# Kernel optimization log

Measured on AMD Instinct MI355X. Metric: run time of the kernel, lower is better.

The kernel has to match this reference:

```python
import jax, jax.numpy as jnp
import numpy as np

N, D, C = 8192, 256, 100
MARGIN = 1.0


def setup_inputs() -> dict:
    key = jax.random.key(0)
    k1, k2 = jax.random.split(key)
    features = jax.random.normal(k1, (N, D), dtype=jnp.float32)
    labels = jax.random.randint(k2, (N,), 0, C, dtype=jnp.int64)
    return {"features": features, "labels": labels}


def _pairwise_dist(f):
    # f: [N, D] L2-normalized rows. Euclidean distance matrix [N, N].
    sq = jnp.sum(f * f, axis=1)  # [N]
    d2 = sq[:, None] + sq[None, :] - 2.0 * (f @ f.T)
    d2 = jnp.maximum(d2, 0.0)
    # safe sqrt: zero distance (incl. diagonal) -> 0 with finite grad
    pos = d2 > 0.0
    return jnp.where(pos, jnp.sqrt(jnp.where(pos, d2, 1.0)), 0.0)


def reference(features, labels):
    # F.normalize(p=2, dim=1)
    norm = jnp.linalg.norm(features, axis=1, keepdims=True)
    f = features / jnp.maximum(norm, 1e-12)

    dist = _pairwise_dist(f)  # [N, N]

    onehot = jax.nn.one_hot(labels, C, dtype=f.dtype)  # [N, C]
    counts = jnp.sum(onehot, axis=0)  # [C]
    # S[a, b] = sum_{i in a, j in b} dist[i, j]
    S = onehot.T @ dist @ onehot  # [C, C]

    # intra: per-class mean over off-diagonal pairs (diag of dist is 0),
    # only classes with count > 1, then mean over those classes
    intra_valid = counts > 1.0
    intra_denom = jnp.where(intra_valid, counts * (counts - 1.0), 1.0)
    intra_per_class = jnp.diag(S) / intra_denom
    n_intra = jnp.sum(intra_valid.astype(f.dtype))
    intra = jnp.where(
        n_intra > 0,
        jnp.sum(jnp.where(intra_valid, intra_per_class, 0.0)) / jnp.maximum(n_intra, 1.0),
        0.0,
    )

    # inter: per class-pair (a < b, both present) mean distance, then mean over pairs
    pair_cnt = counts[:, None] * counts[None, :]
    inter_mat = S / jnp.where(pair_cnt > 0.0, pair_cnt, 1.0)
    present = counts > 0.0
    upper = jnp.triu(jnp.ones((C, C), dtype=bool), k=1)
    pair_mask = upper & present[:, None] & present[None, :]
    n_pairs = jnp.sum(pair_mask.astype(f.dtype))
    inter = jnp.where(
        n_pairs > 0,
        jnp.sum(jnp.where(pair_mask, inter_mat, 0.0)) / jnp.maximum(n_pairs, 1.0),
        1.0,
    )

    loss = jax.nn.relu(intra - inter + MARGIN)
    return loss  # scalar; .mean() of a scalar is itself
```

## Files before the change

kernel.cpp:

```cpp
#include <hip/hip_runtime.h>
#include <math.h>

#define N_ROWS 8192
#define D_DIM  256
#define C_CLS  100
#define BM 128
#define BK 32
#define NSTRIP (N_ROWS / BM)
#define NBLK (NSTRIP * (NSTRIP + 1) / 2)
#define UPK (C_CLS * (C_CLS + 1) / 2)
#define NHB (N_ROWS / 256)
#define MAXSEG 4

typedef __attribute__((ext_vector_type(8))) __bf16 bf16x8;
typedef __attribute__((ext_vector_type(4))) float  floatx4;

__device__ __forceinline__ unsigned short f2bf(float x) {
    unsigned int u = __float_as_uint(x);
    u += 0x7fff + ((u >> 16) & 1);
    return (unsigned short)(u >> 16);
}

__device__ __forceinline__ void gl2lds16(const void* g, void* l) {
    __builtin_amdgcn_global_load_lds(
        (const __attribute__((address_space(1))) void*)g,
        (__attribute__((address_space(3))) void*)l, 16, 0, 0);
}

__global__ void hist_k(const int* __restrict__ labels, int* __restrict__ hist_part) {
    __shared__ int h[C_CLS];
    const int t = threadIdx.x;
    if (t < C_CLS) h[t] = 0;
    __syncthreads();
    atomicAdd(&h[labels[blockIdx.x * 256 + t]], 1);
    __syncthreads();
    if (t < C_CLS) hist_part[blockIdx.x * C_CLS + t] = h[t];
}

__global__ void scan_k(const int* __restrict__ hist_part, int* __restrict__ offs,
                       int* __restrict__ blockoffs, float* __restrict__ Ug) {
    __shared__ int tot[C_CLS];
    const int t = threadIdx.x;
    if (t < C_CLS) {
        int run = 0;
        for (int b = 0; b < NHB; ++b) {
            blockoffs[b * C_CLS + t] = run;
            run += hist_part[b * C_CLS + t];
        }
        tot[t] = run;
    }
    __syncthreads();
    if (t == 0) {
        int run = 0;
        for (int c = 0; c < C_CLS; ++c) { offs[c] = run; run += tot[c]; }
        offs[C_CLS] = run;
    }
    for (int e = t; e < UPK; e += 256) Ug[e] = 0.f;
}

__global__ void scatter_k(const int* __restrict__ labels, const int* __restrict__ offs,
                          const int* __restrict__ blockoffs, int* __restrict__ dest,
                          int* __restrict__ slab) {
    __shared__ int cur[C_CLS];
    const int t = threadIdx.x;
    if (t < C_CLS) cur[t] = offs[t] + blockoffs[blockIdx.x * C_CLS + t];
    __syncthreads();
    const int i  = blockIdx.x * 256 + t;
    const int la = labels[i];
    const int pos = atomicAdd(&cur[la], 1);
    dest[i] = pos;
    slab[pos] = la;
}

__global__ void normalize_k(const float* __restrict__ in, const int* __restrict__ dest,
                            unsigned short* __restrict__ fnb) {
    const int row  = blockIdx.x * 4 + (threadIdx.x >> 6);
    const int lane = threadIdx.x & 63;
    float4 v = ((const float4*)in)[row * 64 + lane];
    float s = v.x * v.x + v.y * v.y + v.z * v.z + v.w * v.w;
#pragma unroll
    for (int o = 32; o > 0; o >>= 1) s += __shfl_xor(s, o, 64);
    const float inv = 1.f / fmaxf(sqrtf(s), 1e-12f);
    const int d = dest[row];
    ushort4 o4;
    o4.x = f2bf(v.x * inv); o4.y = f2bf(v.y * inv);
    o4.z = f2bf(v.z * inv); o4.w = f2bf(v.w * inv);
    ((ushort4*)fnb)[d * 64 + lane] = o4;
}

__global__ __launch_bounds__(256, 4)
void main_k(const unsigned short* __restrict__ fnb, const int* __restrict__ slab,
            const int* __restrict__ offs_g, float* __restrict__ Ug) {
    __shared__ __align__(16) unsigned short As[BM * BK];
    __shared__ __align__(16) unsigned short Bs[BM * BK];
    __shared__ float red[4][MAXSEG * MAXSEG][65];
    __shared__ int soffs[C_CLS + 1];
    __shared__ int meta[4][4];

    const int t = threadIdx.x;

    int b = blockIdx.x, ti = 0, len = NSTRIP;
    while (b >= len) { b -= len; ++ti; --len; }
    const int tj = ti + b;
    const int i0 = ti * BM, j0 = tj * BM;

    if (t < C_CLS + 1) soffs[t] = offs_g[t];
    for (int e = t; e < 4 * MAXSEG * MAXSEG * 65; e += 256) (&red[0][0][0])[e] = 0.f;

    const int lane = t & 63;
    const int w    = t >> 6;
    const int m0 = (w & 1) * 64, n0 = (w >> 1) * 64;
    const int lr = lane & 15, lq = lane >> 4;
    const int swz = (lr >> 1) & 3;

    int aoff[4], boff[4];
#pragma unroll
    for (int mb = 0; mb < 4; ++mb) aoff[mb] = (m0 + mb * 16 + lr) * BK + ((lq ^ swz) * 8);
#pragma unroll
    for (int nb = 0; nb < 4; ++nb) boff[nb] = (n0 + nb * 16 + lr) * BK + ((lq ^ swz) * 8);

    const int s0 = t, s1 = t + 256;
    const int r0 = s0 >> 2, kc0 = (s0 & 3) ^ ((r0 >> 1) & 3);
    const int r1 = s1 >> 2, kc1 = (s1 & 3) ^ ((r1 >> 1) & 3);

    floatx4 acc[4][4];
#pragma unroll
    for (int mb = 0; mb < 4; ++mb)
#pragma unroll
        for (int nb = 0; nb < 4; ++nb) acc[mb][nb] = 0.f;

    for (int k0 = 0; k0 < D_DIM; k0 += BK) {
        __syncthreads();
        gl2lds16(&fnb[(size_t)(i0 + r0) * D_DIM + k0 + kc0 * 8], &As[s0 * 8]);
        gl2lds16(&fnb[(size_t)(i0 + r1) * D_DIM + k0 + kc1 * 8], &As[s1 * 8]);
        gl2lds16(&fnb[(size_t)(j0 + r0) * D_DIM + k0 + kc0 * 8], &Bs[s0 * 8]);
        gl2lds16(&fnb[(size_t)(j0 + r1) * D_DIM + k0 + kc1 * 8], &Bs[s1 * 8]);
        __syncthreads();

        bf16x8 a[4], bb[4];
#pragma unroll
        for (int mb = 0; mb < 4; ++mb) a[mb]  = *(const bf16x8*)&As[aoff[mb]];
#pragma unroll
        for (int nb = 0; nb < 4; ++nb) bb[nb] = *(const bf16x8*)&Bs[boff[nb]];
#pragma unroll
        for (int mb = 0; mb < 4; ++mb)
#pragma unroll
            for (int nb = 0; nb < 4; ++nb)
                acc[mb][nb] = __builtin_amdgcn_mfma_f32_16x16x32_bf16(a[mb], bb[nb], acc[mb][nb], 0, 0, 0);
    }

    const bool diag = (ti == tj);
#pragma unroll
    for (int mb = 0; mb < 4; ++mb)
#pragma unroll
        for (int nb = 0; nb < 4; ++nb)
#pragma unroll
            for (int r = 0; r < 4; ++r) {
                const float g = acc[mb][nb][r];
                float dv = __builtin_amdgcn_sqrtf(fmaxf(2.f - 2.f * g, 0.f));
                const int rt = m0 + mb * 16 + lq * 4 + r;
                const int ct = n0 + nb * 16 + lr;
                if (diag && rt == ct) dv = 0.f;
                acc[mb][nb][r] = dv;
            }

    const int cA0 = __builtin_amdgcn_readfirstlane(slab[i0 + m0]);
    const int cA1 = __builtin_amdgcn_readfirstlane(slab[i0 + m0 + 63]);
    const int cB0 = __builtin_amdgcn_readfirstlane(slab[j0 + n0]);
    const int cB1 = __builtin_amdgcn_readfirstlane(slab[j0 + n0 + 63]);
    const int segsA = cA1 - cA0 + 1, segsB = cB1 - cB0 + 1;
    if (lane == 0) { meta[w][0] = cA0; meta[w][1] = cB0; meta[w][2] = segsA; meta[w][3] = segsB; }
    const float wscale = diag ? 1.f : 2.f;

    float rem[4][4];
#pragma unroll
    for (int mb = 0; mb < 4; ++mb)
#pragma unroll
        for (int r = 0; r < 4; ++r)
            rem[mb][r] = acc[mb][0][r] + acc[mb][1][r] + acc[mb][2][r] + acc[mb][3][r];

    for (int sb = 0; sb < segsB; ++sb) {
        const int cb = cB0 + sb;
        float colsum[4][4];
        if (sb == segsB - 1) {
#pragma unroll
            for (int mb = 0; mb < 4; ++mb)
#pragma unroll
                for (int r = 0; r < 4; ++r) colsum[mb][r] = rem[mb][r];
        } else {
            const int rb0 = max(soffs[cb]     - j0, n0);
            const int rb1 = min(soffs[cb + 1] - j0, n0 + 64);
#pragma unroll
            for (int mb = 0; mb < 4; ++mb)
#pragma unroll
                for (int r = 0; r < 4; ++r) colsum[mb][r] = 0.f;
#pragma unroll
            for (int nb = 0; nb < 4; ++nb) {
                const int ct = n0 + nb * 16 + lr;
                const bool ic = (ct >= rb0) & (ct < rb1);
#pragma unroll
                for (int mb = 0; mb < 4; ++mb)
#pragma unroll
                    for (int r = 0; r < 4; ++r)
                        colsum[mb][r] += ic ? acc[mb][nb][r] : 0.f;
            }
#pragma unroll
            for (int mb = 0; mb < 4; ++mb)
#pragma unroll
                for (int r = 0; r < 4; ++r) rem[mb][r] -= colsum[mb][r];
        }
        for (int sa = 0; sa < segsA; ++sa) {
            const int ca = cA0 + sa;
            const int ra0 = max(soffs[ca]     - i0, m0);
            const int ra1 = min(soffs[ca + 1] - i0, m0 + 64);
            float v = 0.f;
#pragma unroll
            for (int mb = 0; mb < 4; ++mb) {
                const int rtb = m0 + mb * 16 + lq * 4;
#pragma unroll
                for (int r = 0; r < 4; ++r) {
                    const int rt = rtb + r;
                    const bool ir = (rt >= ra0) & (rt < ra1);
                    v += ir ? colsum[mb][r] : 0.f;
                }
            }
            if (sa < MAXSEG && sb < MAXSEG) {
                red[w][sb * MAXSEG + sa][lane] = v;
            } else {
#pragma unroll
                for (int o = 32; o > 0; o >>= 1) v += __shfl_xor(v, o, 64);
                if (lane == 0 && v != 0.f) {
                    const int mn = min(ca, cb), mx = max(ca, cb);
                    atomicAdd(&Ug[mx + ((mn * (2 * C_CLS - 1 - mn)) >> 1)], wscale * v);
                }
            }
        }
    }

    __syncthreads();
    {
        const int combo = t >> 2, q = t & 3;
        const int wv = combo >> 4, sl = combo & 15;
        float s = 0.f;
#pragma unroll
        for (int k = 0; k < 16; ++k) s += red[wv][sl][q * 16 + k];
        s += __shfl_xor(s, 1, 64);
        s += __shfl_xor(s, 2, 64);
        const int sa = sl & (MAXSEG - 1), sb = sl >> 2;
        if (q == 0 && sa < meta[wv][2] && sb < meta[wv][3] && s != 0.f) {
            const int ca = meta[wv][0] + sa, cb = meta[wv][1] + sb;
            const int mn = min(ca, cb), mx = max(ca, cb);
            atomicAdd(&Ug[mx + ((mn * (2 * C_CLS - 1 - mn)) >> 1)], wscale * s);
        }
    }
}

__global__ void finalize_k(const float* __restrict__ U, const int* __restrict__ offs,
                           float* __restrict__ out) {
    __shared__ int   cnt[C_CLS];
    __shared__ float rf[256];
    __shared__ int   ri[256];
    const int t = threadIdx.x;
    if (t < C_CLS) cnt[t] = offs[t + 1] - offs[t];
    __syncthreads();

    float s_intra = 0.f; int n_intra = 0;
    if (t < C_CLS) {
        int c = cnt[t];
        if (c > 1) {
            int idx = t + ((t * (2 * C_CLS - 1 - t)) >> 1);
            s_intra = U[idx] / ((float)c * (float)(c - 1));
            n_intra = 1;
        }
    }
    float s_inter = 0.f; int n_pairs = 0;
    for (int p = t; p < C_CLS * C_CLS; p += 256) {
        int a = p / C_CLS, b2 = p - a * C_CLS;
        if (b2 > a && cnt[a] > 0 && cnt[b2] > 0) {
            int idx = b2 + ((a * (2 * C_CLS - 1 - a)) >> 1);
            s_inter += 0.5f * U[idx] / ((float)cnt[a] * (float)cnt[b2]);
            ++n_pairs;
        }
    }

    rf[t] = s_intra; ri[t] = n_intra; __syncthreads();
    for (int s = 128; s > 0; s >>= 1) {
        if (t < s) { rf[t] += rf[t + s]; ri[t] += ri[t + s]; }
        __syncthreads();
    }
    float intra_sum = rf[0]; int intra_n = ri[0];
    __syncthreads();
    rf[t] = s_inter; ri[t] = n_pairs; __syncthreads();
    for (int s = 128; s > 0; s >>= 1) {
        if (t < s) { rf[t] += rf[t + s]; ri[t] += ri[t + s]; }
        __syncthreads();
    }
    if (t == 0) {
        float inter_sum = rf[0]; int pairs_n = ri[0];
        float intra = (intra_n > 0) ? intra_sum / (float)intra_n : 0.f;
        float inter = (pairs_n > 0) ? inter_sum / (float)pairs_n : 1.f;
        out[0] = fmaxf(intra - inter + 1.0f, 0.f);
    }
}

extern "C" void kernel_launch(void* const* d_in, const int* in_sizes, int n_in,
                              void* d_out, int out_size, void* d_ws, size_t ws_size,
                              hipStream_t stream) {
    const float* feats  = (const float*)d_in[0];
    const int*   labels = (const int*)d_in[1];
    float* out = (float*)d_out;

    char* p = (char*)d_ws;
    unsigned short* fnb = (unsigned short*)p;  p += (size_t)N_ROWS * D_DIM * sizeof(unsigned short);
    int*   slab      = (int*)p;  p += (size_t)N_ROWS * sizeof(int);
    int*   dest      = (int*)p;  p += (size_t)N_ROWS * sizeof(int);
    int*   hist_part = (int*)p;  p += (size_t)NHB * C_CLS * sizeof(int);
    int*   blockoffs = (int*)p;  p += (size_t)NHB * C_CLS * sizeof(int);
    int*   offs      = (int*)p;  p += 128 * sizeof(int);
    float* Ug        = (float*)p;

    hist_k    <<<NHB, 256, 0, stream>>>(labels, hist_part);
    scan_k    <<<1, 256, 0, stream>>>(hist_part, offs, blockoffs, Ug);
    scatter_k <<<NHB, 256, 0, stream>>>(labels, offs, blockoffs, dest, slab);
    normalize_k<<<N_ROWS / 4, 256, 0, stream>>>(feats, dest, fnb);
    main_k    <<<NBLK, 256, 0, stream>>>(fnb, slab, offs, Ug);
    finalize_k<<<1, 256, 0, stream>>>(Ug, offs, out);
}
```

Baseline: 120.4 us.

## Fuse label sort into one kernel and load GEMM operands directly from global

The histogram, scan and scatter kernels are merged into a single 1024-thread block that counts labels, scans the counts and scatters them, cutting two launches and the partial-histogram traffic. The main kernel drops its LDS staging of A/B tiles and per-tile barriers and loads bf16x8 fragments straight from global memory into MFMA operands, relying on L1/L2 for reuse. Launch bounds drop from 4 to 3 waves per SIMD so more registers are available. The explicit zeroing of the red buffer is removed, which may matter if the unseen epilogue relies on it; the single-block sort serialises the work onto one CU.

```diff
diff --git a/kernel.cpp b/kernel.cpp
--- a/kernel.cpp
+++ b/kernel.cpp
@@ -5,11 +5,9 @@
 #define D_DIM  256
 #define C_CLS  100
 #define BM 128
-#define BK 32
 #define NSTRIP (N_ROWS / BM)
 #define NBLK (NSTRIP * (NSTRIP + 1) / 2)
 #define UPK (C_CLS * (C_CLS + 1) / 2)
-#define NHB (N_ROWS / 256)
 #define MAXSEG 4
 
 typedef __attribute__((ext_vector_type(8))) __bf16 bf16x8;
@@ -21,55 +19,38 @@
     return (unsigned short)(u >> 16);
 }
 
-__device__ __forceinline__ void gl2lds16(const void* g, void* l) {
-    __builtin_amdgcn_global_load_lds(
-        (const __attribute__((address_space(1))) void*)g,
-        (__attribute__((address_space(3))) void*)l, 16, 0, 0);
-}
-
-__global__ void hist_k(const int* __restrict__ labels, int* __restrict__ hist_part) {
+__global__ void sort_k(const int* __restrict__ labels, int* __restrict__ dest,
+                       int* __restrict__ slab, int* __restrict__ offs,
+                       float* __restrict__ Ug) {
     __shared__ int h[C_CLS];
+    __shared__ int oS[C_CLS + 1];
+    __shared__ int cur[C_CLS];
     const int t = threadIdx.x;
     if (t < C_CLS) h[t] = 0;
     __syncthreads();
-    atomicAdd(&h[labels[blockIdx.x * 256 + t]], 1);
-    __syncthreads();
-    if (t < C_CLS) hist_part[blockIdx.x * C_CLS + t] = h[t];
-}
-
-__global__ void scan_k(const int* __restrict__ hist_part, int* __restrict__ offs,
-                       int* __restrict__ blockoffs, float* __restrict__ Ug) {
-    __shared__ int tot[C_CLS];
-    const int t = threadIdx.x;
-    if (t < C_CLS) {
-        int run = 0;
-        for (int b = 0; b < NHB; ++b) {
-            blockoffs[b * C_CLS + t] = run;
-            run += hist_part[b * C_CLS + t];
-        }
-        tot[t] = run;
-    }
+    int myl[8];
+#pragma unroll
+    for (int u = 0; u < 8; ++u) myl[u] = labels[t + u * 1024];
+#pragma unroll
+    for (int u = 0; u < 8; ++u) atomicAdd(&h[myl[u]], 1);
     __syncthreads();
     if (t == 0) {
         int run = 0;
-        for (int c = 0; c < C_CLS; ++c) { offs[c] = run; run += tot[c]; }
-        offs[C_CLS] = run;
-    }
-    for (int e = t; e < UPK; e += 256) Ug[e] = 0.f;
-}
-
-__global__ void scatter_k(const int* __restrict__ labels, const int* __restrict__ offs,
-                          const int* __restrict__ blockoffs, int* __restrict__ dest,
-                          int* __restrict__ slab) {
-    __shared__ int cur[C_CLS];
-    const int t = threadIdx.x;
-    if (t < C_CLS) cur[t] = offs[t] + blockoffs[blockIdx.x * C_CLS + t];
-    __syncthreads();
-    const int i  = blockIdx.x * 256 + t;
-    const int la = labels[i];
-    const int pos = atomicAdd(&cur[la], 1);
-    dest[i] = pos;
-    slab[pos] = la;
+        for (int c = 0; c < C_CLS; ++c) { oS[c] = run; run += h[c]; }
+        oS[C_CLS] = run;
+    }
+    __syncthreads();
+    if (t < C_CLS) cur[t] = oS[t];
+    __syncthreads();
+#pragma unroll
+    for (int u = 0; u < 8; ++u) {
+        const int i = t + u * 1024;
+        const int pos = atomicAdd(&cur[myl[u]], 1);
+        dest[i] = pos;
+        slab[pos] = myl[u];
+    }
+    if (t < C_CLS + 1) offs[t] = oS[t];
+    for (int e = t; e < UPK; e += 1024) Ug[e] = 0.f;
 }
 
 __global__ void normalize_k(const float* __restrict__ in, const int* __restrict__ dest,
@@ -88,11 +69,9 @@
     ((ushort4*)fnb)[d * 64 + lane] = o4;
 }
 
-__global__ __launch_bounds__(256, 4)
+__global__ __launch_bounds__(256, 3)
 void main_k(const unsigned short* __restrict__ fnb, const int* __restrict__ slab,
             const int* __restrict__ offs_g, float* __restrict__ Ug) {
-    __shared__ __align__(16) unsigned short As[BM * BK];
-    __shared__ __align__(16) unsigned short Bs[BM * BK];
     __shared__ float red[4][MAXSEG * MAXSEG][65];
     __shared__ int soffs[C_CLS + 1];
     __shared__ int meta[4][4];
@@ -105,23 +84,19 @@
     const int i0 = ti * BM, j0 = tj * BM;
 
     if (t < C_CLS + 1) soffs[t] = offs_g[t];
-    for (int e = t; e < 4 * MAXSEG * MAXSEG * 65; e += 256) (&red[0][0][0])[e] = 0.f;
+    __syncthreads();
 
     const int lane = t & 63;
     const int w    = t >> 6;
     const int m0 = (w & 1) * 64, n0 = (w >> 1) * 64;
     const int lr = lane & 15, lq = lane >> 4;
-    const int swz = (lr >> 1) & 3;
-
-    int aoff[4], boff[4];
-#pragma unroll
-    for (int mb = 0; mb < 4; ++mb) aoff[mb] = (m0 + mb * 16 + lr) * BK + ((lq ^ swz) * 8);
-#pragma unroll
-    for (int nb = 0; nb < 4; ++nb) boff[nb] = (n0 + nb * 16 + lr) * BK + ((lq ^ swz) * 8);
-
-    const int s0 = t, s1 = t + 256;
-    const int r0 = s0 >> 2, kc0 = (s0 & 3) ^ ((r0 >> 1) & 3);
-    const int r1 = s1 >> 2, kc1 = (s1 & 3) ^ ((r1 >> 1) & 3);
+
+    const unsigned short* arow[4];
+    const unsigned short* brow[4];
+#pragma unroll
+    for (int mb = 0; mb < 4; ++mb) arow[mb] = fnb + (size_t)(i0 + m0 + mb * 16 + lr) * D_DIM + lq * 8;
+#pragma unroll
+    for (int nb = 0; nb < 4; ++nb) brow[nb] = fnb + (size_t)(j0 + n0 + nb * 16 + lr) * D_DIM + lq * 8;
 
     floatx4 acc[4][4];
 #pragma unroll
@@ -129,19 +104,13 @@
 #pragma unroll
         for (int nb = 0; nb < 4; ++nb) acc[mb][nb] = 0.f;
 
-    for (int k0 = 0; k0 < D_DIM; k0 += BK) {
-        __syncthreads();
-        gl2lds16(&fnb[(size_t)(i0 + r0) * D_DIM + k0 + kc0 * 8], &As[s0 * 8]);
-        gl2lds16(&fnb[(size_t)(i0 + r1) * D_DIM + k0 + kc1 * 8], &As[s1 * 8]);
-        gl2lds16(&fnb[(size_t)(j0 + r0) * D_DIM + k0 + kc0 * 8], &Bs[s0 * 8]);
-        gl2lds16(&fnb[(size_t)(j0 + r1) * D_DIM + k0 + kc1 * 8], &Bs[s1 * 8]);
-        __syncthreads();
-
+#pragma unroll
+    for (int k0 = 0; k0 < D_DIM; k0 += 32) {
         bf16x8 a[4], bb[4];
 #pragma unroll
-        for (int mb = 0; mb < 4; ++mb) a[mb]  = *(const bf16x8*)&As[aoff[mb]];
-#pragma unroll
-        for (int nb = 0; nb < 4; ++nb) bb[nb] = *(const bf16x8*)&Bs[boff[nb]];
+        for (int mb = 0; mb < 4; ++mb) a[mb]  = *(const bf16x8*)(arow[mb] + k0);
+#pragma unroll
+        for (int nb = 0; nb < 4; ++nb) bb[nb] = *(const bf16x8*)(brow[nb] + k0);
 #pragma unroll
         for (int mb = 0; mb < 4; ++mb)
 #pragma unroll
@@ -312,17 +281,13 @@
 
     char* p = (char*)d_ws;
     unsigned short* fnb = (unsigned short*)p;  p += (size_t)N_ROWS * D_DIM * sizeof(unsigned short);
-    int*   slab      = (int*)p;  p += (size_t)N_ROWS * sizeof(int);
-    int*   dest      = (int*)p;  p += (size_t)N_ROWS * sizeof(int);
-    int*   hist_part = (int*)p;  p += (size_t)NHB * C_CLS * sizeof(int);
-    int*   blockoffs = (int*)p;  p += (size_t)NHB * C_CLS * sizeof(int);
-    int*   offs      = (int*)p;  p += 128 * sizeof(int);
-    float* Ug        = (float*)p;
-
-    hist_k    <<<NHB, 256, 0, stream>>>(labels, hist_part);
-    scan_k    <<<1, 256, 0, stream>>>(hist_part, offs, blockoffs, Ug);
-    scatter_k <<<NHB, 256, 0, stream>>>(labels, offs, blockoffs, dest, slab);
+    int*   slab = (int*)p;  p += (size_t)N_ROWS * sizeof(int);
+    int*   dest = (int*)p;  p += (size_t)N_ROWS * sizeof(int);
+    int*   offs = (int*)p;  p += 128 * sizeof(int);
+    float* Ug   = (float*)p;
+
+    sort_k     <<<1, 1024, 0, stream>>>(labels, dest, slab, offs, Ug);
     normalize_k<<<N_ROWS / 4, 256, 0, stream>>>(feats, dest, fnb);
-    main_k    <<<NBLK, 256, 0, stream>>>(fnb, slab, offs, Ug);
-    finalize_k<<<1, 256, 0, stream>>>(Ug, offs, out);
-}
+    main_k     <<<NBLK, 256, 0, stream>>>(fnb, slab, offs, Ug);
+    finalize_k <<<1, 256, 0, stream>>>(Ug, offs, out);
+}
```

Measured after the change: 156.2 us. 29.7% more time.
